# Kernel optimization log

Hardware: AMD Instinct MI355X
Metric: run time of the kernel (lower is better)

## Reference

```python
import jax, jax.numpy as jnp
import numpy as np
from jax import lax

B, T, C, H, K = 2, 4096, 2048, 16, 4
D = C // H
EPS = 1e-5


def _ln(x, g, b):
    m = x.mean(-1, keepdims=True)
    v = ((x - m) ** 2).mean(-1, keepdims=True)
    return (x - m) / jnp.sqrt(v + EPS) * g + b


def _l2norm(x):
    n = jnp.sqrt(jnp.sum(x * x, axis=-1, keepdims=True))
    return x / jnp.maximum(n, 1e-12)


def setup_inputs() -> dict:
    key = jax.random.key(0)
    ks = jax.random.split(key, 10)
    s = 1.0 / np.sqrt(C)
    x = jax.random.normal(ks[0], (B, T, C), jnp.float32)
    Wq = jax.random.normal(ks[1], (C, C), jnp.float32) * s
    Wk = jax.random.normal(ks[2], (C, C), jnp.float32) * s
    Wv = jax.random.normal(ks[3], (C, C), jnp.float32) * s
    Wo = jax.random.normal(ks[4], (C, C), jnp.float32) * s
    conv_w = jax.random.normal(ks[5], (C, 1, K), jnp.float32) * 0.5  # depthwise (O, I/g, K)
    conv_b = jnp.zeros((C,), jnp.float32)
    Wig = jax.random.normal(ks[6], (C, C), jnp.float32) * 0.02
    big = jnp.full((C,), -2.0, jnp.float32)  # gate_init_bias
    Wog = jax.random.normal(ks[7], (C, C), jnp.float32) * s
    bog = jnp.zeros((C,), jnp.float32)
    Wgam = jax.random.normal(ks[8], (H, C), jnp.float32) * 0.02
    decays = 1.0 - np.exp(np.linspace(np.log(1 - 0.9), np.log(1 - 0.9999), H))
    bgam = jnp.asarray(np.log(decays / (1 - decays)), jnp.float32)
    vn_g = jnp.ones((D,), jnp.float32); vn_b = jnp.zeros((D,), jnp.float32)
    mn_g = jnp.ones((D,), jnp.float32); mn_b = jnp.zeros((D,), jnp.float32)
    gn_g = jnp.ones((C,), jnp.float32); gn_b = jnp.zeros((C,), jnp.float32)
    return dict(x=x, Wq=Wq, Wk=Wk, Wv=Wv, Wo=Wo, conv_w=conv_w, conv_b=conv_b,
                Wig=Wig, big=big, Wog=Wog, bog=bog, Wgam=Wgam, bgam=bgam,
                vn_g=vn_g, vn_b=vn_b, mn_g=mn_g, mn_b=mn_b, gn_g=gn_g, gn_b=gn_b)


def reference(x, Wq, Wk, Wv, Wo, conv_w, conv_b, Wig, big, Wog, bog, Wgam, bgam,
              vn_g, vn_b, mn_g, mn_b, gn_g, gn_b):
    # Causal depthwise conv1d over time
    xt = jnp.transpose(x, (0, 2, 1))                     # [B,C,T]
    xp = jnp.pad(xt, ((0, 0), (0, 0), (K - 1, 0)))
    xc = lax.conv_general_dilated(xp, conv_w, (1,), 'VALID', feature_group_count=C)
    xc = xc + conv_b[None, :, None]
    x_conv = jax.nn.silu(jnp.transpose(xc, (0, 2, 1)))   # [B,T,C]

    q = _l2norm((x @ Wq.T).reshape(B, T, H, D))
    k = _l2norm((x @ Wk.T).reshape(B, T, H, D))
    v = _ln((x @ Wv.T).reshape(B, T, H, D), vn_g, vn_b)
    i_gate = jax.nn.sigmoid(x_conv @ Wig.T + big).reshape(B, T, H, D)
    gamma = jax.nn.sigmoid(x_conv @ Wgam.T + bgam).reshape(B, T, H, 1)

    # Gated linear recurrence: mem_t = gamma_t * mem_{t-1} + i_t * k_t * v_t
    kv = i_gate * k * v
    def combine(c1, c2):
        a1, b1 = c1
        a2, b2 = c2
        return a1 * a2, a2 * b1 + b2
    _, mem = lax.associative_scan(combine, (gamma, kv), axis=1)  # mem: [B,T,H,D]

    mem_out = _ln(mem, mn_g, mn_b)
    out = (mem_out * q).reshape(B * T, H, D)
    # GroupNorm(num_groups=H) over channels
    m = out.mean(-1, keepdims=True)
    var = ((out - m) ** 2).mean(-1, keepdims=True)
    out = (out - m) / jnp.sqrt(var + EPS)
    out = out * gn_g.reshape(H, D) + gn_b.reshape(H, D)
    out = out.reshape(B, T, C)
    out = out * jax.nn.sigmoid(x_conv @ Wog.T + bog)
    return out @ Wo.T
```

## Files before the change

kernel.cpp:

```cpp
#include <hip/hip_runtime.h>
#include <cstdint>
#include <cstddef>

using u16 = unsigned short;
using bf16x8 = __attribute__((ext_vector_type(8))) __bf16;
using f32x4  = __attribute__((ext_vector_type(4))) float;

constexpr int Bb = 2, Tt = 4096, Cc = 2048, Hh = 16, Dd = 128;
constexpr int Mm = Bb * Tt;
constexpr int CHK = 32;
constexpr int NCH = Tt / CHK;
constexpr float EPSf = 1e-5f;

__device__ __forceinline__ u16 f2bf(float f) {
  union { float f; uint32_t u; } v; v.f = f;
  return (u16)((v.u + 0x7fffu + ((v.u >> 16) & 1u)) >> 16);
}
__device__ __forceinline__ float bf2f(u16 h) {
  union { uint32_t u; float f; } v; v.u = ((uint32_t)h) << 16;
  return v.f;
}
__device__ __forceinline__ float sig_(float z) { return 1.f / (1.f + __expf(-z)); }
__device__ __forceinline__ float wred(float v) {
#pragma unroll
  for (int m = 32; m; m >>= 1) v += __shfl_xor(v, m);
  return v;
}
__device__ __forceinline__ void glds16(const u16* g, u16* l) {
  __builtin_amdgcn_global_load_lds(
      (const __attribute__((address_space(1))) unsigned int*)g,
      (__attribute__((address_space(3))) unsigned int*)l, 16, 0, 0);
}
__device__ __forceinline__ void bar_() { asm volatile("s_barrier" ::: "memory"); }

__global__ void la_conv(const float* __restrict__ x, const float* __restrict__ cw,
                        const float* __restrict__ cb, u16* __restrict__ xbf,
                        u16* __restrict__ xconv) {
  int i4 = blockIdx.x * 256 + threadIdx.x;
  int c4 = i4 & (Cc / 4 - 1);
  int bt = i4 >> 9;
  int t = bt & (Tt - 1);
  const float4* x4 = (const float4*)x;
  float4 xv = x4[i4];
  float4 xm1 = t >= 1 ? x4[i4 - Cc / 4] : make_float4(0, 0, 0, 0);
  float4 xm2 = t >= 2 ? x4[i4 - Cc / 2] : make_float4(0, 0, 0, 0);
  float4 xm3 = t >= 3 ? x4[i4 - 3 * Cc / 4] : make_float4(0, 0, 0, 0);
  ushort4 ob; ushort4 oc;
  const float4* cw4 = (const float4*)cw;
  float vv[4]  = {xv.x, xv.y, xv.z, xv.w};
  float v1[4]  = {xm1.x, xm1.y, xm1.z, xm1.w};
  float v2[4]  = {xm2.x, xm2.y, xm2.z, xm2.w};
  float v3[4]  = {xm3.x, xm3.y, xm3.z, xm3.w};
  u16 rb[4], rc[4];
#pragma unroll
  for (int j = 0; j < 4; j++) {
    int c = c4 * 4 + j;
    float4 w = cw4[c];
    float acc = cb[c] + w.w * vv[j] + w.z * v1[j] + w.y * v2[j] + w.x * v3[j];
    rb[j] = f2bf(vv[j]);
    rc[j] = f2bf(acc * sig_(acc));
  }
  ob.x = rb[0]; ob.y = rb[1]; ob.z = rb[2]; ob.w = rb[3];
  oc.x = rc[0]; oc.y = rc[1]; oc.z = rc[2]; oc.w = rc[3];
  ((ushort4*)xbf)[i4] = ob;
  ((ushort4*)xconv)[i4] = oc;
}

__global__ void la_cvt5(const float* w0, const float* w1, const float* w2,
                        const float* w3, const float* w4,
                        u16* o0, u16* o1, u16* o2, u16* o3, u16* o4, int n4each) {
  int i = blockIdx.x * 256 + threadIdx.x;
  int seg = i / n4each;
  int off = i - seg * n4each;
  const float* src = seg == 0 ? w0 : seg == 1 ? w1 : seg == 2 ? w2 : seg == 3 ? w3 : w4;
  u16* dst = seg == 0 ? o0 : seg == 1 ? o1 : seg == 2 ? o2 : seg == 3 ? o3 : o4;
  float4 v = ((const float4*)src)[off];
  ushort4 o;
  o.x = f2bf(v.x); o.y = f2bf(v.y); o.z = f2bf(v.z); o.w = f2bf(v.w);
  ((ushort4*)dst)[off] = o;
}

__global__ void la_cvt(const float* __restrict__ in, u16* __restrict__ out, int n4) {
  int i = blockIdx.x * 256 + threadIdx.x;
  if (i < n4) {
    float4 v = ((const float4*)in)[i];
    ushort4 o;
    o.x = f2bf(v.x); o.y = f2bf(v.y); o.z = f2bf(v.z); o.w = f2bf(v.w);
    ((ushort4*)out)[i] = o;
  }
}

__global__ __launch_bounds__(256) void la_gamma(
    const u16* __restrict__ xconv, const float* __restrict__ Wg,
    const float* __restrict__ bg, float* __restrict__ gam) {
  __shared__ u16 wlds[Hh * Cc];
  for (int i = threadIdx.x; i < Hh * Cc / 4; i += 256) {
    float4 v = ((const float4*)Wg)[i];
    ushort4 o;
    o.x = f2bf(v.x); o.y = f2bf(v.y); o.z = f2bf(v.z); o.w = f2bf(v.w);
    ((ushort4*)wlds)[i] = o;
  }
  __syncthreads();
  const int wave = threadIdx.x >> 6, lane = threadIdx.x & 63;
  const int row0 = blockIdx.x * 16 + wave * 4;
#pragma unroll
  for (int r = 0; r < 4; r++) {
    const int row = row0 + r;
    const u16* xr = xconv + (size_t)row * Cc + lane * 8;
    bf16x8 xv[4];
#pragma unroll
    for (int it = 0; it < 4; it++) xv[it] = *(const bf16x8*)(xr + it * 512);
#pragma unroll
    for (int h = 0; h < 16; h++) {
      const u16* wr = wlds + h * Cc + lane * 8;
      float acc = 0.f;
#pragma unroll
      for (int it = 0; it < 4; it++) {
        bf16x8 wv = *(const bf16x8*)(wr + it * 512);
#pragma unroll
        for (int e = 0; e < 8; e++) acc += (float)xv[it][e] * (float)wv[e];
      }
      acc = wred(acc);
      if (lane == 0) gam[row * Hh + h] = sig_(acc + bg[h]);
    }
  }
}

__global__ void la_prep(const u16* pq, const u16* pk, const u16* pv, const u16* pig,
                        const float* __restrict__ vng, const float* __restrict__ vnb,
                        const float* __restrict__ bigv, u16* qo, u16* kvo) {
  const int wave = threadIdx.x >> 6, lane = threadIdx.x & 63;
  const int p = blockIdx.x * 4 + wave;
  const int row = p >> 4, h = p & 15;
  const int d0 = lane * 2;
  const size_t base = (size_t)row * Cc + h * Dd + d0;
  uint32_t uq = *(const uint32_t*)(pq + base);
  uint32_t uk = *(const uint32_t*)(pk + base);
  uint32_t uv = *(const uint32_t*)(pv + base);
  uint32_t ui = *(const uint32_t*)(pig + base);
  float q0 = bf2f((u16)uq), q1 = bf2f((u16)(uq >> 16));
  float k0 = bf2f((u16)uk), k1 = bf2f((u16)(uk >> 16));
  float v0 = bf2f((u16)uv), v1 = bf2f((u16)(uv >> 16));
  float i0 = bf2f((u16)ui), i1 = bf2f((u16)(ui >> 16));
  float qs = wred(q0*q0 + q1*q1);
  float ks = wred(k0*k0 + k1*k1);
  float s1 = wred(v0 + v1);
  float s2 = wred(v0*v0 + v1*v1);
  float qn = 1.f / fmaxf(sqrtf(qs), 1e-12f);
  float kn = 1.f / fmaxf(sqrtf(ks), 1e-12f);
  float mu = s1 * (1.f / Dd);
  float var = s2 * (1.f / Dd) - mu * mu;
  float rs = rsqrtf(var + EPSf);
  int c0 = h * Dd + d0;
  float vh0 = (v0 - mu) * rs * vng[d0]     + vnb[d0];
  float vh1 = (v1 - mu) * rs * vng[d0 + 1] + vnb[d0 + 1];
  float ig0 = sig_(i0 + bigv[c0]);
  float ig1 = sig_(i1 + bigv[c0 + 1]);
  float kv0 = ig0 * (k0 * kn) * vh0;
  float kv1 = ig1 * (k1 * kn) * vh1;
  *(uint32_t*)(qo + base)  = (uint32_t)f2bf(q0 * qn) | ((uint32_t)f2bf(q1 * qn) << 16);
  *(uint32_t*)(kvo + base) = (uint32_t)f2bf(kv0)     | ((uint32_t)f2bf(kv1) << 16);
}

__global__ void la_scan1(u16* __restrict__ kv, float* __restrict__ gam,
                         float* __restrict__ Ebuf) {
  const int wave = threadIdx.x >> 6, lane = threadIdx.x & 63;
  const int p = blockIdx.x * 4 + wave;
  const int bh = p >> 7, c = p & (NCH - 1);
  const int b = bh >> 4, h = bh & 15;
  const int t0 = c * CHK;
  const size_t rbase = (size_t)b * Tt + t0;
  const size_t base = rbase * Cc + h * Dd + lane * 2;
  float* gp = gam + rbase * Hh + h;
  float m0 = 0.f, m1 = 0.f, cg = 1.f;
#pragma unroll 4
  for (int t = 0; t < CHK; t++) {
    float g = gp[(size_t)t * Hh];
    cg *= g;
    uint32_t u = *(const uint32_t*)(kv + base + (size_t)t * Cc);
    m0 = fmaf(g, m0, bf2f((u16)u));
    m1 = fmaf(g, m1, bf2f((u16)(u >> 16)));
    *(uint32_t*)(kv + base + (size_t)t * Cc) =
        (uint32_t)f2bf(m0) | ((uint32_t)f2bf(m1) << 16);
    if (lane == 0) gp[(size_t)t * Hh] = cg;
  }
  float2 e; e.x = m0; e.y = m1;
  *(float2*)&Ebuf[(size_t)p * Dd + lane * 2] = e;
}

__global__ void la_scan2(const float* __restrict__ Ebuf, const float* __restrict__ cumg,
                         float* __restrict__ carry) {
  const int bh = blockIdx.x;
  const int b = bh >> 4, h = bh & 15;
  const int lane = threadIdx.x;
  float S0 = 0.f, S1 = 0.f;
  for (int c = 0; c < NCH; c++) {
    size_t idx = ((size_t)bh * NCH + c) * Dd + lane * 2;
    float2 s; s.x = S0; s.y = S1;
    *(float2*)&carry[idx] = s;
    float2 E = *(const float2*)&Ebuf[idx];
    float P = cumg[((size_t)b * Tt + c * CHK + CHK - 1) * Hh + h];
    S0 = fmaf(P, S0, E.x);
    S1 = fmaf(P, S1, E.y);
  }
}

__global__ void la_post(const u16* mem, const u16* q, const u16* ogp,
                        const float* __restrict__ cumg, const float* __restrict__ carry,
                        const float* __restrict__ mng, const float* __restrict__ mnb,
                        const float* __restrict__ gng, const float* __restrict__ gnb,
                        const float* __restrict__ bog, u16* outb) {
  const int wave = threadIdx.x >> 6, lane = threadIdx.x & 63;
  const int p = blockIdx.x * 4 + wave;
  const int row = p >> 4, h = p & 15;
  const int b = row >> 12, t = row & (Tt - 1), ch = t >> 5;
  const int d0 = lane * 2;
  const size_t base = (size_t)row * Cc + h * Dd + d0;
  uint32_t um = *(const uint32_t*)(mem + base);
  uint32_t uq = *(const uint32_t*)(q + base);
  uint32_t uo = *(const uint32_t*)(ogp + base);
  float cg = cumg[p];
  float2 cr = *(const float2*)&carry[(((size_t)(b * Hh + h)) * NCH + ch) * Dd + d0];
  float m0 = fmaf(cg, cr.x, bf2f((u16)um));
  float m1 = fmaf(cg, cr.y, bf2f((u16)(um >> 16)));
  float q0 = bf2f((u16)uq), q1 = bf2f((u16)(uq >> 16));
  float g0 = bf2f((u16)uo), g1 = bf2f((u16)(uo >> 16));
  float s1 = wred(m0 + m1);
  float s2 = wred(m0*m0 + m1*m1);
  float mu = s1 * (1.f / Dd);
  float var = s2 * (1.f / Dd) - mu * mu;
  float rs = rsqrtf(var + EPSf);
  int c0 = h * Dd + d0;
  float mo0 = (m0 - mu) * rs * mng[d0]     + mnb[d0];
  float mo1 = (m1 - mu) * rs * mng[d0 + 1] + mnb[d0 + 1];
  float o0 = mo0 * q0, o1 = mo1 * q1;
  float t1 = wred(o0 + o1);
  float t2 = wred(o0*o0 + o1*o1);
  float mu2 = t1 * (1.f / Dd);
  float var2 = t2 * (1.f / Dd) - mu2 * mu2;
  float rs2 = rsqrtf(var2 + EPSf);
  float y0 = (o0 - mu2) * rs2 * gng[c0]     + gnb[c0];
  float y1 = (o1 - mu2) * rs2 * gng[c0 + 1] + gnb[c0 + 1];
  y0 *= sig_(g0 + bog[c0]);
  y1 *= sig_(g1 + bog[c0 + 1]);
  *(uint32_t*)(outb + base) = (uint32_t)f2bf(y0) | ((uint32_t)f2bf(y1) << 16);
}

#define STAGE(t, j) do {                                                        \
    const u16* _s = (((j) == 0 || (j) == 2) ? Ab : Wb)                          \
                    + (((j) == 1 || (j) == 2) ? (size_t)128 * K : (size_t)0)    \
                    + soff + (size_t)(t) * 64;                                  \
    u16* _d = dbase + ((((t) & 1) * 4 + (j)) * 8192);                           \
    glds16(_s, _d);                                                             \
    glds16(_s + 8 * (size_t)K, _d + 512);                                       \
  } while (0)

#define LDFRAG(DST, NFR, SLOT, RBASE) do {                                      \
    _Pragma("unroll")                                                           \
    for (int _i = 0; _i < (NFR); ++_i)                                          \
      _Pragma("unroll")                                                         \
      for (int _ks = 0; _ks < 2; ++_ks)                                         \
        DST[_i][_ks] = *(const bf16x8*)&(SLOT)[((RBASE) + _i * 16) * 64 +       \
                         ((((lane >> 4) + _ks * 4) ^ x7) * 8)];                 \
  } while (0)

#define MM16(QM, QN, AA, BB) do {                                               \
    __builtin_amdgcn_s_setprio(1);                                              \
    _Pragma("unroll")                                                           \
    for (int _mi = 0; _mi < 4; ++_mi)                                           \
      _Pragma("unroll")                                                         \
      for (int _ni = 0; _ni < 2; ++_ni)                                         \
        _Pragma("unroll")                                                       \
        for (int _ks = 0; _ks < 2; ++_ks)                                       \
          acc[QM][QN][_mi][_ni] = __builtin_amdgcn_mfma_f32_16x16x32_bf16(      \
              AA[_mi][_ks], BB[_ni][_ks], acc[QM][QN][_mi][_ni], 0, 0, 0);      \
    __builtin_amdgcn_s_setprio(0);                                              \
  } while (0)

#define MM16_ARD(QM, QN, AA, BB, RSLOT) do {                                    \
    __builtin_amdgcn_s_setprio(1);                                              \
    _Pragma("unroll")                                                           \
    for (int _mi = 0; _mi < 4; ++_mi) {                                         \
      _Pragma("unroll")                                                         \
      for (int _ni = 0; _ni < 2; ++_ni)                                         \
        _Pragma("unroll")                                                       \
        for (int _ks = 0; _ks < 2; ++_ks)                                       \
          acc[QM][QN][_mi][_ni] = __builtin_amdgcn_mfma_f32_16x16x32_bf16(      \
              AA[_mi][_ks], BB[_ni][_ks], acc[QM][QN][_mi][_ni], 0, 0, 0);      \
      _Pragma("unroll")                                                         \
      for (int _ks = 0; _ks < 2; ++_ks)                                         \
        AA[_mi][_ks] = *(const bf16x8*)&(RSLOT)[((ra) + _mi * 16) * 64 +        \
                         ((((lane >> 4) + _ks * 4) ^ x7) * 8)];                 \
    }                                                                           \
    __builtin_amdgcn_s_setprio(0);                                              \
  } while (0)

template <int OUT_BF16>
__global__ __launch_bounds__(512, 2)
void la_gemm(const u16* __restrict__ A,
             const u16* __restrict__ W0, const u16* __restrict__ W1,
             const u16* __restrict__ W2,
             void* __restrict__ C0, void* __restrict__ C1, void* __restrict__ C2,
             int K) {
  __shared__ u16 lds[8 * 8192];
  const int tid  = threadIdx.x;
  const int lane = tid & 63;
  const int wv   = tid >> 6;
  const int wm = wv >> 2;
  const int wn = wv & 3;
  const int fm = lane & 15;
  const int x7 = fm & 7;
  const int seg = blockIdx.x >> 3;
  const int bn = (blockIdx.x & 7) * 256;
  const int bm = blockIdx.y * 256;
  const u16* W = seg == 0 ? W0 : (seg == 1 ? W1 : W2);
  void* Co = seg == 0 ? C0 : (seg == 1 ? C1 : C2);

  const u16* Ab = A + (size_t)bm * K;
  const u16* Wb = W + (size_t)bn * K;
  const size_t soff = (size_t)(wv * 16 + (lane >> 3)) * K
                      + (size_t)(((lane & 7) ^ (lane >> 3)) * 8);
  u16* const dbase = lds + wv * 1024;
  const int nkt = K >> 6;
  const int ra = wm * 64 + fm;
  const int rb = wn * 32 + fm;

  f32x4 acc[2][2][4][2] = {};
  bf16x8 af[4][2], b0f[2][2], b1f[2][2];

  STAGE(0, 0); STAGE(0, 1); STAGE(0, 2); STAGE(0, 3);
  __builtin_amdgcn_sched_barrier(0);
  STAGE(1, 2); STAGE(1, 1); STAGE(1, 3);
  asm volatile("s_waitcnt vmcnt(6)" ::: "memory");
  bar_();
  LDFRAG(b1f, 2, lds + 1 * 8192, rb);
  LDFRAG(af, 4, lds + 2 * 8192, ra);

  for (int kt = 0; kt < nkt; ++kt) {
    u16* const cur = lds + (kt & 1) * 4 * 8192;
    u16* const nxt = lds + ((kt & 1) ^ 1) * 4 * 8192;

    bar_();
    LDFRAG(b0f, 2, cur + 3 * 8192, rb);
    if (kt + 1 < nkt) STAGE(kt + 1, 0);
    __builtin_amdgcn_sched_barrier(0);
    MM16(1, 1, af, b1f);

    bar_();
    if (kt + 2 < nkt) STAGE(kt + 2, 2);
    __builtin_amdgcn_sched_barrier(0);
    MM16_ARD(1, 0, af, b0f, cur + 0 * 8192);

    bar_();
    if (kt + 2 < nkt) STAGE(kt + 2, 1);
    __builtin_amdgcn_sched_barrier(0);
    MM16(0, 1, af, b1f);
    if (kt < nkt - 2)       asm volatile("s_waitcnt vmcnt(4)" ::: "memory");
    else if (kt == nkt - 2) asm volatile("s_waitcnt vmcnt(0)" ::: "memory");

    bar_();
    if (kt + 1 < nkt) {
      LDFRAG(b1f, 2, nxt + 1 * 8192, rb);
      if (kt + 2 < nkt) STAGE(kt + 2, 3);
      __builtin_amdgcn_sched_barrier(0);
      MM16_ARD(0, 0, af, b0f, nxt + 2 * 8192);
    } else {
      __builtin_amdgcn_sched_barrier(0);
      MM16(0, 0, af, b0f);
    }
  }

  const int cr = (lane >> 4) * 4;
  const int cc = lane & 15;
#pragma unroll
  for (int qm = 0; qm < 2; ++qm)
#pragma unroll
    for (int qn = 0; qn < 2; ++qn)
#pragma unroll
      for (int mi = 0; mi < 4; ++mi)
#pragma unroll
        for (int ni = 0; ni < 2; ++ni)
#pragma unroll
          for (int r = 0; r < 4; ++r) {
            size_t off = (size_t)(bm + qm * 128 + wm * 64 + mi * 16 + cr + r) * Cc
                         + (bn + qn * 128 + wn * 32 + ni * 16 + cc);
            if (OUT_BF16) ((u16*)Co)[off] = f2bf(acc[qm][qn][mi][ni][r]);
            else          ((float*)Co)[off] = acc[qm][qn][mi][ni][r];
          }
}

extern "C" void kernel_launch(void* const* d_in, const int* in_sizes, int n_in,
                              void* d_out, int out_size, void* d_ws, size_t ws_size,
                              hipStream_t stream) {
  (void)in_sizes; (void)n_in; (void)out_size; (void)ws_size;
  const float* x    = (const float*)d_in[0];
  const float* Wq   = (const float*)d_in[1];
  const float* Wk   = (const float*)d_in[2];
  const float* Wv   = (const float*)d_in[3];
  const float* Wo   = (const float*)d_in[4];
  const float* cw   = (const float*)d_in[5];
  const float* cb   = (const float*)d_in[6];
  const float* Wig  = (const float*)d_in[7];
  const float* big  = (const float*)d_in[8];
  const float* Wog  = (const float*)d_in[9];
  const float* bog  = (const float*)d_in[10];
  const float* Wgam = (const float*)d_in[11];
  const float* bgam = (const float*)d_in[12];
  const float* vng  = (const float*)d_in[13];
  const float* vnb  = (const float*)d_in[14];
  const float* mng  = (const float*)d_in[15];
  const float* mnb  = (const float*)d_in[16];
  const float* gng  = (const float*)d_in[17];
  const float* gnb  = (const float*)d_in[18];

  char* ws = (char*)d_ws;
  const size_t NB = (size_t)Mm * Cc * 2;
  u16* xbf   = (u16*)(ws + 0 * NB);
  u16* xconv = (u16*)(ws + 1 * NB);
  u16* preq  = (u16*)(ws + 2 * NB);
  u16* prek  = (u16*)(ws + 3 * NB);
  u16* prev  = (u16*)(ws + 4 * NB);
  u16* preig = (u16*)(ws + 5 * NB);
  u16* wbf   = (u16*)(ws + 6 * NB);
  float* gam = (float*)(ws + 6 * NB + (size_t)Cc * Cc * 2);
  const size_t WE = (size_t)Cc * Cc;
  u16* wk_bf  = preig;
  u16* wv_bf  = preig + WE;
  u16* wig_bf = preig + 2 * WE;
  u16* wog_bf = preig + 3 * WE;
  float* Ebuf  = (float*)preig;
  float* carry = (float*)(preig + 1024 * 1024);
  u16* ogscr = (u16*)d_out;

  const int WN4 = Cc * Cc / 4;
  dim3 blk(256);
  dim3 gblk(512);

  la_conv<<<Mm * Cc / 4 / 256, blk, 0, stream>>>(x, cw, cb, xbf, xconv);

  la_cvt5<<<5 * WN4 / 256, blk, 0, stream>>>(Wq, Wk, Wv, Wig, Wog,
                                             wbf, wk_bf, wv_bf, wig_bf, wog_bf, WN4);

  la_gemm<1><<<dim3(24, Mm / 256), gblk, 0, stream>>>(
      xbf, wbf, wk_bf, wv_bf, (void*)preq, (void*)prek, (void*)prev, Cc);

  la_cvt<<<WN4 / 256, blk, 0, stream>>>(Wo, wbf, WN4);

  la_gemm<1><<<dim3(16, Mm / 256), gblk, 0, stream>>>(
      xconv, wig_bf, wog_bf, wog_bf, (void*)xbf, (void*)ogscr, (void*)ogscr, Cc);

  la_gamma<<<Mm / 16, blk, 0, stream>>>(xconv, Wgam, bgam, gam);

  la_prep<<<Mm * Hh / 4, blk, 0, stream>>>(preq, prek, prev, xbf,
                                           vng, vnb, big, preq, prek);

  la_scan1<<<Bb * Hh * NCH / 4, blk, 0, stream>>>(prek, gam, Ebuf);
  la_scan2<<<Bb * Hh, dim3(64), 0, stream>>>(Ebuf, gam, carry);

  la_post<<<Mm * Hh / 4, blk, 0, stream>>>(prek, preq, ogscr, gam, carry,
                                           mng, mnb, gng, gnb, bog, xbf);

  la_gemm<0><<<dim3(8, Mm / 256), gblk, 0, stream>>>(
      xbf, wbf, wbf, wbf, d_out, d_out, d_out, Cc);
}
```

Measured before the change: 758.3 us.

## Interleave B-fragment LDS reads into MFMA loop and reorder GEMM staging

Adds an MM16_BRD macro that reloads the B fragments from LDS between MFMAs, so the standalone LDFRAG of b1f before the last quadrant is no longer needed. The staging order of the four LDS slots is rotated (1,2,3,0) and the wait counts are rebalanced across the phases of the main k-loop. The intent is to hide LDS read latency behind MFMA work and keep more global loads in flight. This makes the vmcnt accounting more intricate, and a wrong count could cause stalls or data races.

```diff
diff --git a/kernel.cpp b/kernel.cpp
--- a/kernel.cpp
+++ b/kernel.cpp
@@ -295,6 +295,24 @@
     __builtin_amdgcn_s_setprio(0);                                              \
   } while (0)
 
+#define MM16_BRD(QM, QN, AA, BB, RSLOT) do {                                    \
+    __builtin_amdgcn_s_setprio(1);                                              \
+    _Pragma("unroll")                                                           \
+    for (int _ni = 0; _ni < 2; ++_ni) {                                         \
+      _Pragma("unroll")                                                         \
+      for (int _mi = 0; _mi < 4; ++_mi)                                         \
+        _Pragma("unroll")                                                       \
+        for (int _ks = 0; _ks < 2; ++_ks)                                       \
+          acc[QM][QN][_mi][_ni] = __builtin_amdgcn_mfma_f32_16x16x32_bf16(      \
+              AA[_mi][_ks], BB[_ni][_ks], acc[QM][QN][_mi][_ni], 0, 0, 0);      \
+      _Pragma("unroll")                                                         \
+      for (int _ks = 0; _ks < 2; ++_ks)                                         \
+        BB[_ni][_ks] = *(const bf16x8*)&(RSLOT)[((rb) + _ni * 16) * 64 +        \
+                         ((((lane >> 4) + _ks * 4) ^ x7) * 8)];                 \
+    }                                                                           \
+    __builtin_amdgcn_s_setprio(0);                                              \
+  } while (0)
+
 template <int OUT_BF16>
 __global__ __launch_bounds__(512, 2)
 void la_gemm(const u16* __restrict__ A,
@@ -328,9 +346,9 @@
   f32x4 acc[2][2][4][2] = {};
   bf16x8 af[4][2], b0f[2][2], b1f[2][2];
 
-  STAGE(0, 0); STAGE(0, 1); STAGE(0, 2); STAGE(0, 3);
+  STAGE(0, 1); STAGE(0, 2); STAGE(0, 3); STAGE(0, 0);
   __builtin_amdgcn_sched_barrier(0);
-  STAGE(1, 2); STAGE(1, 1); STAGE(1, 3);
+  STAGE(1, 1); STAGE(1, 2); STAGE(1, 3);
   asm volatile("s_waitcnt vmcnt(6)" ::: "memory");
   bar_();
   LDFRAG(b1f, 2, lds + 1 * 8192, rb);
@@ -347,27 +365,25 @@
     MM16(1, 1, af, b1f);
 
     bar_();
+    if (kt + 2 < nkt) STAGE(kt + 2, 1);
+    __builtin_amdgcn_sched_barrier(0);
+    MM16_ARD(1, 0, af, b0f, cur + 0 * 8192);
+    if (kt < nkt - 2)  asm volatile("s_waitcnt vmcnt(6)" ::: "memory");
+    else               asm volatile("s_waitcnt vmcnt(4)" ::: "memory");
+
+    bar_();
     if (kt + 2 < nkt) STAGE(kt + 2, 2);
     __builtin_amdgcn_sched_barrier(0);
-    MM16_ARD(1, 0, af, b0f, cur + 0 * 8192);
+    if (kt + 1 < nkt) MM16_BRD(0, 1, af, b1f, nxt + 1 * 8192);
+    else              MM16(0, 1, af, b1f);
 
     bar_();
-    if (kt + 2 < nkt) STAGE(kt + 2, 1);
+    if (kt + 2 < nkt) STAGE(kt + 2, 3);
     __builtin_amdgcn_sched_barrier(0);
-    MM16(0, 1, af, b1f);
-    if (kt < nkt - 2)       asm volatile("s_waitcnt vmcnt(4)" ::: "memory");
+    if (kt + 1 < nkt) MM16_ARD(0, 0, af, b0f, nxt + 2 * 8192);
+    else              MM16(0, 0, af, b0f);
+    if (kt < nkt - 2)       asm volatile("s_waitcnt vmcnt(6)" ::: "memory");
     else if (kt == nkt - 2) asm volatile("s_waitcnt vmcnt(0)" ::: "memory");
-
-    bar_();
-    if (kt + 1 < nkt) {
-      LDFRAG(b1f, 2, nxt + 1 * 8192, rb);
-      if (kt + 2 < nkt) STAGE(kt + 2, 3);
-      __builtin_amdgcn_sched_barrier(0);
-      MM16_ARD(0, 0, af, b0f, nxt + 2 * 8192);
-    } else {
-      __builtin_amdgcn_sched_barrier(0);
-      MM16(0, 0, af, b0f);
-    }
   }
 
   const int cr = (lane >> 4) * 4;
```

Result: no change. 756.5 us (-0.2%).

## Fuse prep normalization into chunk scan and q l2norm into post kernel

Applied to the files above, without the earlier changes.

Removes the la_prep kernel. The k l2norm, v layernorm and input-gate sigmoid now run inside la_scan1 while it reads the raw projections, and the q l2norm moves into la_post. This drops one full elementwise pass that read four activation tensors and wrote two back. la_scan1 and la_scan2 now batch their loads 8 steps ahead to hide latency, and la_gamma processes 32 rows per block so the LDS weight conversion is amortized over more rows. The cost is extra reductions inside the serial scan loop and higher register pressure.

```diff
diff --git a/kernel.cpp b/kernel.cpp
--- a/kernel.cpp
+++ b/kernel.cpp
@@ -102,9 +102,9 @@
   }
   __syncthreads();
   const int wave = threadIdx.x >> 6, lane = threadIdx.x & 63;
-  const int row0 = blockIdx.x * 16 + wave * 4;
-#pragma unroll
-  for (int r = 0; r < 4; r++) {
+  const int row0 = blockIdx.x * 32 + wave * 8;
+#pragma unroll
+  for (int r = 0; r < 8; r++) {
     const int row = row0 + r;
     const u16* xr = xconv + (size_t)row * Cc + lane * 8;
     bf16x8 xv[4];
@@ -126,44 +126,11 @@
   }
 }
 
-__global__ void la_prep(const u16* pq, const u16* pk, const u16* pv, const u16* pig,
-                        const float* __restrict__ vng, const float* __restrict__ vnb,
-                        const float* __restrict__ bigv, u16* qo, u16* kvo) {
-  const int wave = threadIdx.x >> 6, lane = threadIdx.x & 63;
-  const int p = blockIdx.x * 4 + wave;
-  const int row = p >> 4, h = p & 15;
-  const int d0 = lane * 2;
-  const size_t base = (size_t)row * Cc + h * Dd + d0;
-  uint32_t uq = *(const uint32_t*)(pq + base);
-  uint32_t uk = *(const uint32_t*)(pk + base);
-  uint32_t uv = *(const uint32_t*)(pv + base);
-  uint32_t ui = *(const uint32_t*)(pig + base);
-  float q0 = bf2f((u16)uq), q1 = bf2f((u16)(uq >> 16));
-  float k0 = bf2f((u16)uk), k1 = bf2f((u16)(uk >> 16));
-  float v0 = bf2f((u16)uv), v1 = bf2f((u16)(uv >> 16));
-  float i0 = bf2f((u16)ui), i1 = bf2f((u16)(ui >> 16));
-  float qs = wred(q0*q0 + q1*q1);
-  float ks = wred(k0*k0 + k1*k1);
-  float s1 = wred(v0 + v1);
-  float s2 = wred(v0*v0 + v1*v1);
-  float qn = 1.f / fmaxf(sqrtf(qs), 1e-12f);
-  float kn = 1.f / fmaxf(sqrtf(ks), 1e-12f);
-  float mu = s1 * (1.f / Dd);
-  float var = s2 * (1.f / Dd) - mu * mu;
-  float rs = rsqrtf(var + EPSf);
-  int c0 = h * Dd + d0;
-  float vh0 = (v0 - mu) * rs * vng[d0]     + vnb[d0];
-  float vh1 = (v1 - mu) * rs * vng[d0 + 1] + vnb[d0 + 1];
-  float ig0 = sig_(i0 + bigv[c0]);
-  float ig1 = sig_(i1 + bigv[c0 + 1]);
-  float kv0 = ig0 * (k0 * kn) * vh0;
-  float kv1 = ig1 * (k1 * kn) * vh1;
-  *(uint32_t*)(qo + base)  = (uint32_t)f2bf(q0 * qn) | ((uint32_t)f2bf(q1 * qn) << 16);
-  *(uint32_t*)(kvo + base) = (uint32_t)f2bf(kv0)     | ((uint32_t)f2bf(kv1) << 16);
-}
-
-__global__ void la_scan1(u16* __restrict__ kv, float* __restrict__ gam,
-                         float* __restrict__ Ebuf) {
+__global__ void la_scan1(const u16* pk, const u16* __restrict__ pv,
+                         const u16* __restrict__ pig,
+                         const float* __restrict__ vng, const float* __restrict__ vnb,
+                         const float* __restrict__ bigv,
+                         u16* mem, float* gam, float* __restrict__ Ebuf) {
   const int wave = threadIdx.x >> 6, lane = threadIdx.x & 63;
   const int p = blockIdx.x * 4 + wave;
   const int bh = p >> 7, c = p & (NCH - 1);
@@ -172,17 +139,52 @@
   const size_t rbase = (size_t)b * Tt + t0;
   const size_t base = rbase * Cc + h * Dd + lane * 2;
   float* gp = gam + rbase * Hh + h;
+  const int d0 = lane * 2;
+  const int c0 = h * Dd + d0;
+  const float vg0 = vng[d0], vg1 = vng[d0 + 1];
+  const float vb0 = vnb[d0], vb1 = vnb[d0 + 1];
+  const float bg0 = bigv[c0], bg1 = bigv[c0 + 1];
   float m0 = 0.f, m1 = 0.f, cg = 1.f;
-#pragma unroll 4
-  for (int t = 0; t < CHK; t++) {
-    float g = gp[(size_t)t * Hh];
-    cg *= g;
-    uint32_t u = *(const uint32_t*)(kv + base + (size_t)t * Cc);
-    m0 = fmaf(g, m0, bf2f((u16)u));
-    m1 = fmaf(g, m1, bf2f((u16)(u >> 16)));
-    *(uint32_t*)(kv + base + (size_t)t * Cc) =
-        (uint32_t)f2bf(m0) | ((uint32_t)f2bf(m1) << 16);
-    if (lane == 0) gp[(size_t)t * Hh] = cg;
+  for (int tb = 0; tb < CHK; tb += 8) {
+    uint32_t uk[8], uv[8], ui[8]; float g[8];
+#pragma unroll
+    for (int j = 0; j < 8; j++) {
+      size_t bb = base + (size_t)(tb + j) * Cc;
+      uk[j] = *(const uint32_t*)(pk + bb);
+      uv[j] = *(const uint32_t*)(pv + bb);
+      ui[j] = *(const uint32_t*)(pig + bb);
+      g[j] = gp[(size_t)(tb + j) * Hh];
+    }
+#pragma unroll
+    for (int j = 0; j < 8; j++) {
+      float k0 = bf2f((u16)uk[j]), k1 = bf2f((u16)(uk[j] >> 16));
+      float v0 = bf2f((u16)uv[j]), v1 = bf2f((u16)(uv[j] >> 16));
+      float i0 = bf2f((u16)ui[j]), i1 = bf2f((u16)(ui[j] >> 16));
+      float ks = k0 * k0 + k1 * k1;
+      float s1 = v0 + v1;
+      float s2 = v0 * v0 + v1 * v1;
+#pragma unroll
+      for (int m = 32; m; m >>= 1) {
+        ks += __shfl_xor(ks, m);
+        s1 += __shfl_xor(s1, m);
+        s2 += __shfl_xor(s2, m);
+      }
+      float kn = 1.f / fmaxf(sqrtf(ks), 1e-12f);
+      float mu = s1 * (1.f / Dd);
+      float var = s2 * (1.f / Dd) - mu * mu;
+      float rs = rsqrtf(var + EPSf);
+      float vh0 = (v0 - mu) * rs * vg0 + vb0;
+      float vh1 = (v1 - mu) * rs * vg1 + vb1;
+      float kv0 = sig_(i0 + bg0) * (k0 * kn) * vh0;
+      float kv1 = sig_(i1 + bg1) * (k1 * kn) * vh1;
+      float gg = g[j];
+      cg *= gg;
+      m0 = fmaf(gg, m0, kv0);
+      m1 = fmaf(gg, m1, kv1);
+      size_t bb = base + (size_t)(tb + j) * Cc;
+      *(uint32_t*)(mem + bb) = (uint32_t)f2bf(m0) | ((uint32_t)f2bf(m1) << 16);
+      if (lane == 0) gp[(size_t)(tb + j) * Hh] = cg;
+    }
   }
   float2 e; e.x = m0; e.y = m1;
   *(float2*)&Ebuf[(size_t)p * Dd + lane * 2] = e;
@@ -194,18 +196,26 @@
   const int b = bh >> 4, h = bh & 15;
   const int lane = threadIdx.x;
   float S0 = 0.f, S1 = 0.f;
-  for (int c = 0; c < NCH; c++) {
-    size_t idx = ((size_t)bh * NCH + c) * Dd + lane * 2;
-    float2 s; s.x = S0; s.y = S1;
-    *(float2*)&carry[idx] = s;
-    float2 E = *(const float2*)&Ebuf[idx];
-    float P = cumg[((size_t)b * Tt + c * CHK + CHK - 1) * Hh + h];
-    S0 = fmaf(P, S0, E.x);
-    S1 = fmaf(P, S1, E.y);
-  }
-}
-
-__global__ void la_post(const u16* mem, const u16* q, const u16* ogp,
+  for (int cb = 0; cb < NCH; cb += 8) {
+    float2 E[8]; float P[8];
+#pragma unroll
+    for (int j = 0; j < 8; j++) {
+      size_t idx = ((size_t)bh * NCH + cb + j) * Dd + lane * 2;
+      E[j] = *(const float2*)&Ebuf[idx];
+      P[j] = cumg[((size_t)b * Tt + (cb + j) * CHK + CHK - 1) * Hh + h];
+    }
+#pragma unroll
+    for (int j = 0; j < 8; j++) {
+      size_t idx = ((size_t)bh * NCH + cb + j) * Dd + lane * 2;
+      float2 s; s.x = S0; s.y = S1;
+      *(float2*)&carry[idx] = s;
+      S0 = fmaf(P[j], S0, E[j].x);
+      S1 = fmaf(P[j], S1, E[j].y);
+    }
+  }
+}
+
+__global__ void la_post(const u16* mem, const u16* qp, const u16* ogp,
                         const float* __restrict__ cumg, const float* __restrict__ carry,
                         const float* __restrict__ mng, const float* __restrict__ mnb,
                         const float* __restrict__ gng, const float* __restrict__ gnb,
@@ -217,7 +227,7 @@
   const int d0 = lane * 2;
   const size_t base = (size_t)row * Cc + h * Dd + d0;
   uint32_t um = *(const uint32_t*)(mem + base);
-  uint32_t uq = *(const uint32_t*)(q + base);
+  uint32_t uq = *(const uint32_t*)(qp + base);
   uint32_t uo = *(const uint32_t*)(ogp + base);
   float cg = cumg[p];
   float2 cr = *(const float2*)&carry[(((size_t)(b * Hh + h)) * NCH + ch) * Dd + d0];
@@ -225,6 +235,9 @@
   float m1 = fmaf(cg, cr.y, bf2f((u16)(um >> 16)));
   float q0 = bf2f((u16)uq), q1 = bf2f((u16)(uq >> 16));
   float g0 = bf2f((u16)uo), g1 = bf2f((u16)(uo >> 16));
+  float qs = wred(q0 * q0 + q1 * q1);
+  float qn = 1.f / fmaxf(sqrtf(qs), 1e-12f);
+  q0 *= qn; q1 *= qn;
   float s1 = wred(m0 + m1);
   float s2 = wred(m0*m0 + m1*m1);
   float mu = s1 * (1.f / Dd);
@@ -449,12 +462,10 @@
   la_gemm<1><<<dim3(16, Mm / 256), gblk, 0, stream>>>(
       xconv, wig_bf, wog_bf, wog_bf, (void*)xbf, (void*)ogscr, (void*)ogscr, Cc);
 
-  la_gamma<<<Mm / 16, blk, 0, stream>>>(xconv, Wgam, bgam, gam);
-
-  la_prep<<<Mm * Hh / 4, blk, 0, stream>>>(preq, prek, prev, xbf,
-                                           vng, vnb, big, preq, prek);
-
-  la_scan1<<<Bb * Hh * NCH / 4, blk, 0, stream>>>(prek, gam, Ebuf);
+  la_gamma<<<Mm / 32, blk, 0, stream>>>(xconv, Wgam, bgam, gam);
+
+  la_scan1<<<Bb * Hh * NCH / 4, blk, 0, stream>>>(prek, prev, xbf,
+                                                  vng, vnb, big, prek, gam, Ebuf);
   la_scan2<<<Bb * Hh, dim3(64), 0, stream>>>(Ebuf, gam, carry);
 
   la_post<<<Mm * Hh / 4, blk, 0, stream>>>(prek, preq, ogscr, gam, carry,
```

Measured after the change: 989.1 us. 1.3x slower.
